# Optimization experiments

Measured on AMD Instinct MI355X. Metric: run time of the kernel, lower is better.

The kernel has to match this reference:

```python
import jax, jax.numpy as jnp
import numpy as np

B, S, HID = 1, 4096, 2048
H, KVH, D = 8, 4, 256
SW = 1024          # sliding window
EPS = 1e-6
NEG = -1e30


def _rmsnorm(x, w=None, eps=EPS):
    # torch nn.RMSNorm: x / sqrt(mean(x^2) + eps) * weight
    y = x * jax.lax.rsqrt(jnp.mean(x * x, axis=-1, keepdims=True) + eps)
    return y * w if w is not None else y


def _rotate_half(x):
    x1, x2 = jnp.split(x, 2, axis=-1)
    return jnp.concatenate([-x2, x1], axis=-1)


def _rope(x, cos, sin):
    # x: [B,S,H,D]; cos/sin: [B,S,rot] -> [B,S,1,rot]; rot == D here (no pass-through)
    c = cos[:, :, None, :]
    s = sin[:, :, None, :]
    return x * c + _rotate_half(x) * s


def setup_inputs() -> dict:
    key = jax.random.key(0)
    ks = jax.random.split(key, 9)
    return {
        "hidden_states": jax.random.normal(ks[0], (B, S, HID), jnp.float32),
        "cos": jax.random.uniform(ks[1], (B, S, D), jnp.float32),
        "sin": jax.random.uniform(ks[2], (B, S, D), jnp.float32),
        "q_w": jax.random.normal(ks[3], (H * D, HID), jnp.float32) * 0.02,
        "k_w": jax.random.normal(ks[4], (KVH * D, HID), jnp.float32) * 0.02,
        "v_w": jax.random.normal(ks[5], (KVH * D, HID), jnp.float32) * 0.02,
        "o_w": jax.random.normal(ks[6], (HID, H * D), jnp.float32) * 0.02,
        "q_norm_w": jnp.ones((D,), jnp.float32),
        "k_norm_w": jnp.ones((D,), jnp.float32),
    }


def reference(hidden_states, cos, sin, q_w, k_w, v_w, o_w, q_norm_w, k_norm_w):
    b, s, _ = hidden_states.shape
    # Projections (no bias), reshape to [B,S,heads,D]
    q = (hidden_states @ q_w.T).reshape(b, s, H, D)
    k = (hidden_states @ k_w.T).reshape(b, s, KVH, D)
    v = (hidden_states @ v_w.T).reshape(b, s, KVH, D)
    # per-head RMSNorm (v_norm has no affine), then RoPE on q/k
    q = _rope(_rmsnorm(q, q_norm_w), cos, sin)
    k = _rope(_rmsnorm(k, k_norm_w), cos, sin)
    v = _rmsnorm(v)
    # flatten(0,1): packed tokens T = B*S
    T = b * s
    q = q.reshape(T, H, D).transpose(1, 0, 2)          # [H,T,D]
    k = k.reshape(T, KVH, D).transpose(1, 0, 2)        # [KVH,T,D]
    v = v.reshape(T, KVH, D).transpose(1, 0, 2)
    # GQA: repeat_interleave kv heads
    rep = H // KVH
    k = jnp.repeat(k, rep, axis=0)                     # [H,T,D]
    v = jnp.repeat(v, rep, axis=0)
    # causal + sliding-window mask (allowed: i-SW < j <= i), scale=1.0
    i = jnp.arange(T)[:, None]
    j = jnp.arange(T)[None, :]
    allowed = (j <= i) & ((i - j) < SW)                # [T,T] bool
    scores = jnp.einsum("htd,hsd->hts", q, k)          # [H,T,T]
    scores = jnp.where(allowed[None], scores, NEG)
    p = jax.nn.softmax(scores, axis=-1)
    out = jnp.einsum("hts,hsd->htd", p, v)             # [H,T,D]
    out = out.transpose(1, 0, 2).reshape(b, s, H * D)
    return out @ o_w.T
```

## Files before the change

kernel.cpp:

```cpp
#include <hip/hip_runtime.h>
#include <stdint.h>

typedef __bf16 bf16x8 __attribute__((ext_vector_type(8)));
typedef __bf16 bf16x4 __attribute__((ext_vector_type(4)));
typedef _Float16 f16x8 __attribute__((ext_vector_type(8)));
typedef _Float16 f16x4 __attribute__((ext_vector_type(4)));
typedef float f32x4v __attribute__((ext_vector_type(4)));

__device__ __forceinline__ void async_copy16(const void* gptr, void* ldsptr) {
  __builtin_amdgcn_global_load_lds(
      (const __attribute__((address_space(1))) void*)gptr,
      (__attribute__((address_space(3))) void*)ldsptr,
      16, 0, 0);
}

__global__ __launch_bounds__(256) void cvt_split_f16(
    const float* __restrict__ src, _Float16* __restrict__ hi,
    _Float16* __restrict__ lo, int n4) {
  const int i = blockIdx.x * 256 + threadIdx.x;
  if (i < n4) {
    const float4 v = ((const float4*)src)[i];
    float vv[4] = {v.x, v.y, v.z, v.w};
    f16x4 h, l;
    for (int j = 0; j < 4; ++j) {
      h[j] = (_Float16)vv[j];
      l[j] = (_Float16)(vv[j] - (float)h[j]);
    }
    ((f16x4*)hi)[i] = h;
    ((f16x4*)lo)[i] = l;
  }
}

__global__ __launch_bounds__(256) void cvt_f16(
    const float* __restrict__ src, _Float16* __restrict__ hi, int n4) {
  const int i = blockIdx.x * 256 + threadIdx.x;
  if (i < n4) {
    const float4 v = ((const float4*)src)[i];
    f16x4 h = {(_Float16)v.x, (_Float16)v.y, (_Float16)v.z, (_Float16)v.w};
    ((f16x4*)hi)[i] = h;
  }
}

__global__ __launch_bounds__(256, 4) void gemm_qkv(
    const _Float16* __restrict__ Ah, const _Float16* __restrict__ Al,
    const _Float16* __restrict__ Bh, float* __restrict__ C) {
  const int K = 2048, ldc = 4096;
  __shared__ __align__(16) _Float16 Ash[128 * 32];
  __shared__ __align__(16) _Float16 Asl[128 * 32];
  __shared__ __align__(16) _Float16 Bsh[128 * 32];
  const int bid = blockIdx.x;
  const int xcd = bid & 7, c = bid >> 3;
  const int m0 = (c >> 2) * 128, n0 = (xcd * 4 + (c & 3)) * 128;
  const int tid = threadIdx.x;
  const int wid = tid >> 6, lane = tid & 63, l15 = lane & 15, quad = lane >> 4;
  const int wm = wid >> 1, wn = wid & 1;

  f32x4v acc[4][4] = {};

  for (int kb = 0; kb < K; kb += 32) {
    for (int it = 0; it < 2; ++it) {
      const int cc = (wid * 2 + it) * 64 + lane;
      const int row = cc >> 2;
      const int sc = (cc & 3) ^ ((row >> 1) & 3);
      const size_t ao = (size_t)(m0 + row) * K + kb + sc * 8;
      const size_t bo = (size_t)(n0 + row) * K + kb + sc * 8;
      const int dst = (wid * 2 + it) * 512;
      async_copy16(Ah + ao, &Ash[dst]);
      async_copy16(Al + ao, &Asl[dst]);
      async_copy16(Bh + bo, &Bsh[dst]);
    }
    __syncthreads();
    f16x8 afh[4], afl[4], bfh[4];
    for (int mt = 0; mt < 4; ++mt) {
      const int r = wm * 64 + mt * 16 + l15;
      const int o = r * 32 + ((quad ^ ((r >> 1) & 3)) * 8);
      afh[mt] = *(const f16x8*)&Ash[o];
      afl[mt] = *(const f16x8*)&Asl[o];
    }
    for (int nt = 0; nt < 4; ++nt) {
      const int r = wn * 64 + nt * 16 + l15;
      const int o = r * 32 + ((quad ^ ((r >> 1) & 3)) * 8);
      bfh[nt] = *(const f16x8*)&Bsh[o];
    }
    for (int mt = 0; mt < 4; ++mt)
      for (int nt = 0; nt < 4; ++nt) {
        acc[mt][nt] = __builtin_amdgcn_mfma_f32_16x16x32_f16(afh[mt], bfh[nt], acc[mt][nt], 0, 0, 0);
        acc[mt][nt] = __builtin_amdgcn_mfma_f32_16x16x32_f16(afl[mt], bfh[nt], acc[mt][nt], 0, 0, 0);
      }
    __syncthreads();
  }
  for (int mt = 0; mt < 4; ++mt)
    for (int nt = 0; nt < 4; ++nt) {
      const int row = m0 + wm * 64 + mt * 16 + quad * 4;
      const int col = n0 + wn * 64 + nt * 16 + l15;
      for (int r = 0; r < 4; ++r)
        C[(size_t)(row + r) * ldc + col] = acc[mt][nt][r];
    }
}

__global__ __launch_bounds__(64) void norm_rope(
    const float* __restrict__ qkv, const float* __restrict__ cosb,
    const float* __restrict__ sinb, const float* __restrict__ qnw,
    const float* __restrict__ knw,
    _Float16* __restrict__ qh, _Float16* __restrict__ ql,
    _Float16* __restrict__ kh, _Float16* __restrict__ vT) {
  const int s = blockIdx.x, c = blockIdx.y, lane = threadIdx.x;
  const int d0 = lane * 4;
  const float4 xv = *(const float4*)(qkv + (size_t)s * 4096 + c * 256 + d0);
  float v[4] = {xv.x, xv.y, xv.z, xv.w};
  float ss = v[0] * v[0] + v[1] * v[1] + v[2] * v[2] + v[3] * v[3];
  for (int off = 1; off < 64; off <<= 1) ss += __shfl_xor(ss, off);
  const float rn = rsqrtf(ss * (1.0f / 256.0f) + 1e-6f);
  if (c < 12) {
    const float* w = (c < 8) ? qnw : knw;
    float y[4], yp[4];
    for (int j = 0; j < 4; ++j) y[j] = v[j] * rn * w[d0 + j];
    for (int j = 0; j < 4; ++j) yp[j] = __shfl_xor(y[j], 32);
    for (int j = 0; j < 4; ++j) {
      const int d = d0 + j;
      const float rot = (d < 128) ? -yp[j] : yp[j];
      y[j] = y[j] * cosb[s * 256 + d] + rot * sinb[s * 256 + d];
    }
    if (c < 8) {
      const size_t o = ((size_t)c * 4096 + s) * 256 + d0;
      f16x4 hv, lv;
      for (int j = 0; j < 4; ++j) {
        hv[j] = (_Float16)y[j];
        lv[j] = (_Float16)(y[j] - (float)hv[j]);
      }
      *(f16x4*)(qh + o) = hv;
      *(f16x4*)(ql + o) = lv;
    } else {
      const size_t o = ((size_t)(c - 8) * 4096 + s) * 256 + d0;
      f16x4 hv;
      for (int j = 0; j < 4; ++j) hv[j] = (_Float16)y[j];
      *(f16x4*)(kh + o) = hv;
    }
  } else {
    const int kvh = c - 12;
    for (int j = 0; j < 4; ++j)
      vT[(size_t)(kvh * 256 + d0 + j) * 4096 + s] = (_Float16)(v[j] * rn);
  }
}

__global__ __launch_bounds__(512, 2) void attn_mfma(
    const _Float16* __restrict__ Qh_, const _Float16* __restrict__ Ql_,
    const _Float16* __restrict__ Kh_, const _Float16* __restrict__ VT,
    _Float16* __restrict__ Aout) {
  const int S = 4096, D = 256;
  const int bid = blockIdx.y * 32 + blockIdx.x;
  const int swz = (bid & 7) * 32 + (bid >> 3);
  const int h = swz >> 5;
  const int q0 = (swz & 31) * 128;
  const int tid = threadIdx.x;
  const int wid = tid >> 6, lane = tid & 63, l15 = lane & 15, quad = lane >> 4;
  const int kv = h >> 1;

  __shared__ __align__(16) _Float16 Ksh[2][32 * 256];
  __shared__ __align__(16) _Float16 Vs[2][256 * 32];
  __shared__ __align__(16) _Float16 P[8][16][32];

  const _Float16* Khh = Kh_ + (size_t)kv * S * D;
  const _Float16* Vh = VT + (size_t)kv * D * S;

  auto stage = [&](int buf, int kt) {
    for (int set = 0; set < 2; ++set) {
      const int n = set * 512 + wid * 64 + lane;
      const int row = n >> 5, c = n & 31;
      const int sc = c ^ (row & 7);
      const size_t go = (size_t)(kt + row) * D + sc * 8;
      const int dst = (set * 512 + wid * 64) * 8;
      async_copy16(Khh + go, &Ksh[buf][dst]);
      const int dim = n >> 2, kc = n & 3;
      const size_t vo = (size_t)dim * S + kt + (kc ^ ((dim >> 1) & 3)) * 8;
      async_copy16(Vh + vo, &Vs[buf][dst]);
    }
  };

  f16x8 qfh[8], qfl[8];
  {
    const size_t qoff =
        (size_t)h * S * D + (size_t)(q0 + wid * 16 + l15) * D + quad * 8;
    for (int ks = 0; ks < 8; ++ks) {
      qfh[ks] = *(const f16x8*)(Qh_ + qoff + ks * 32);
      qfl[ks] = *(const f16x8*)(Ql_ + qoff + ks * 32);
    }
  }

  f32x4v O[16] = {};
  float mrow[4] = {-1e30f, -1e30f, -1e30f, -1e30f};
  float lrow[4] = {0.f, 0.f, 0.f, 0.f};

  const int lo = (q0 >= 1024) ? (q0 - 1024) : 0;
  const int hi = q0 + 96;
  const int iqmin = q0 + wid * 16;
  const int iqmax = iqmin + 15;

  stage(0, lo);
  __syncthreads();
  int cur = 0;

  for (int kt = lo; kt <= hi; kt += 32) {
    if (kt + 32 <= hi) stage(cur ^ 1, kt + 32);
    const bool active = (kt <= iqmax) && (kt + 31 >= iqmin - 1023);
    if (active) {
      f32x4v sa[2] = {};
      for (int nt = 0; nt < 2; ++nt) {
        const int row = nt * 16 + l15;
        const int rxk = row & 7;
        for (int ks = 0; ks < 8; ++ks) {
          const int c = (ks * 4 + quad) ^ rxk;
          const f16x8 kh8 = *(const f16x8*)&Ksh[cur][row * 256 + c * 8];
          sa[nt] = __builtin_amdgcn_mfma_f32_16x16x32_f16(qfh[ks], kh8, sa[nt], 0, 0, 0);
          sa[nt] = __builtin_amdgcn_mfma_f32_16x16x32_f16(qfl[ks], kh8, sa[nt], 0, 0, 0);
        }
      }
      float al[4];
      for (int r = 0; r < 4; ++r) {
        const int i = q0 + wid * 16 + quad * 4 + r;
        float mx = -1e30f;
        for (int nt = 0; nt < 2; ++nt) {
          const int j = kt + nt * 16 + l15;
          const float svv = ((j <= i) && (i - j < 1024)) ? sa[nt][r] : -1e30f;
          sa[nt][r] = svv;
          mx = fmaxf(mx, svv);
        }
        for (int off = 1; off < 16; off <<= 1) mx = fmaxf(mx, __shfl_xor(mx, off));
        const float mn = fmaxf(mrow[r], mx);
        al[r] = __expf(mrow[r] - mn);
        float ps = 0.f;
        const int prow = quad * 4 + r;
        const int px = (prow >> 1) & 3;
        for (int nt = 0; nt < 2; ++nt) {
          const float p = (mn <= -1e29f) ? 0.f : __expf(sa[nt][r] - mn);
          const int pc = (nt * 2 + (l15 >> 3)) ^ px;
          P[wid][prow][pc * 8 + (l15 & 7)] = (_Float16)p;
          ps += p;
        }
        for (int off = 1; off < 16; off <<= 1) ps += __shfl_xor(ps, off);
        lrow[r] = lrow[r] * al[r] + ps;
        mrow[r] = mn;
      }
      for (int nt2 = 0; nt2 < 16; ++nt2)
        for (int r = 0; r < 4; ++r) O[nt2][r] *= al[r];
      __asm__ volatile("s_waitcnt lgkmcnt(0)" ::: "memory");
      __builtin_amdgcn_sched_barrier(0);
      const int prx = (l15 >> 1) & 3;
      const f16x8 pf = *(const f16x8*)&P[wid][l15][(quad ^ prx) * 8];
      for (int nt2 = 0; nt2 < 16; ++nt2) {
        const int dim = nt2 * 16 + l15;
        const int vq = quad ^ ((dim >> 1) & 3);
        const f16x8 vf = *(const f16x8*)&Vs[cur][(dim * 4 + vq) * 8];
        O[nt2] = __builtin_amdgcn_mfma_f32_16x16x32_f16(pf, vf, O[nt2], 0, 0, 0);
      }
    }
    __syncthreads();
    cur ^= 1;
  }
  for (int nt2 = 0; nt2 < 16; ++nt2)
    for (int r = 0; r < 4; ++r) {
      const float o = O[nt2][r] / lrow[r];
      Aout[(size_t)(q0 + wid * 16 + quad * 4 + r) * 2048 + h * 256 + nt2 * 16 + l15] = (_Float16)o;
    }
}

__global__ __launch_bounds__(256, 4) void gemm_out(
    const _Float16* __restrict__ A, const _Float16* __restrict__ B,
    float* __restrict__ C) {
  const int K = 2048, ldc = 2048;
  __shared__ __align__(16) _Float16 As[128 * 32];
  __shared__ __align__(16) _Float16 Bs[128 * 32];
  const int bid = blockIdx.x;
  const int xcd = bid & 7, c = bid >> 3;
  const int m0 = (c >> 1) * 128, n0 = (xcd * 2 + (c & 1)) * 128;
  const int tid = threadIdx.x;
  const int wid = tid >> 6, lane = tid & 63, l15 = lane & 15, quad = lane >> 4;
  const int wm = wid >> 1, wn = wid & 1;

  f32x4v acc[4][4] = {};

  for (int kb = 0; kb < K; kb += 32) {
    for (int it = 0; it < 2; ++it) {
      const int cc = (wid * 2 + it) * 64 + lane;
      const int row = cc >> 2;
      const int sc = (cc & 3) ^ ((row >> 1) & 3);
      const size_t ao = (size_t)(m0 + row) * K + kb + sc * 8;
      const size_t bo = (size_t)(n0 + row) * K + kb + sc * 8;
      const int dst = (wid * 2 + it) * 512;
      async_copy16(A + ao, &As[dst]);
      async_copy16(B + bo, &Bs[dst]);
    }
    __syncthreads();
    f16x8 af[4], bfr[4];
    for (int mt = 0; mt < 4; ++mt) {
      const int r = wm * 64 + mt * 16 + l15;
      af[mt] = *(const f16x8*)&As[r * 32 + ((quad ^ ((r >> 1) & 3)) * 8)];
    }
    for (int nt = 0; nt < 4; ++nt) {
      const int r = wn * 64 + nt * 16 + l15;
      bfr[nt] = *(const f16x8*)&Bs[r * 32 + ((quad ^ ((r >> 1) & 3)) * 8)];
    }
    for (int mt = 0; mt < 4; ++mt)
      for (int nt = 0; nt < 4; ++nt)
        acc[mt][nt] = __builtin_amdgcn_mfma_f32_16x16x32_f16(af[mt], bfr[nt], acc[mt][nt], 0, 0, 0);
    __syncthreads();
  }
  for (int mt = 0; mt < 4; ++mt)
    for (int nt = 0; nt < 4; ++nt) {
      const int row = m0 + wm * 64 + mt * 16 + quad * 4;
      const int col = n0 + wn * 64 + nt * 16 + l15;
      for (int r = 0; r < 4; ++r)
        C[(size_t)(row + r) * ldc + col] = acc[mt][nt][r];
    }
}

extern "C" void kernel_launch(void* const* d_in, const int* in_sizes, int n_in,
                              void* d_out, int out_size, void* d_ws, size_t ws_size,
                              hipStream_t stream) {
  const float* hidden = (const float*)d_in[0];
  const float* cosb   = (const float*)d_in[1];
  const float* sinb   = (const float*)d_in[2];
  const float* qw     = (const float*)d_in[3];
  const float* kw     = (const float*)d_in[4];
  const float* vw     = (const float*)d_in[5];
  const float* ow     = (const float*)d_in[6];
  const float* qnw    = (const float*)d_in[7];
  const float* knw    = (const float*)d_in[8];
  float* out = (float*)d_out;

  const size_t MB = 1048576;
  char* ws = (char*)d_ws;
  float*    qkvf = (float*)ws;
  _Float16* attn = (_Float16*)ws;
  _Float16* hh   = (_Float16*)(ws + 64 * MB);
  _Float16* hl   = (_Float16*)(ws + 80 * MB);
  _Float16* wh   = (_Float16*)(ws + 96 * MB);
  _Float16* qh   = (_Float16*)(ws + 64 * MB);
  _Float16* ql   = (_Float16*)(ws + 80 * MB);
  _Float16* kh   = (_Float16*)(ws + 96 * MB);
  _Float16* vT   = (_Float16*)(ws + 104 * MB);
  _Float16* owh  = (_Float16*)(ws + 112 * MB);

  cvt_split_f16<<<dim3(8192), 256, 0, stream>>>(hidden, hh, hl, 2097152);
  cvt_f16<<<dim3(4096), 256, 0, stream>>>(qw, wh, 1048576);
  cvt_f16<<<dim3(2048), 256, 0, stream>>>(kw, wh + 4194304, 524288);
  cvt_f16<<<dim3(2048), 256, 0, stream>>>(vw, wh + 6291456, 524288);
  cvt_f16<<<dim3(4096), 256, 0, stream>>>(ow, owh, 1048576);

  gemm_qkv<<<dim3(1024), 256, 0, stream>>>(hh, hl, wh, qkvf);
  norm_rope<<<dim3(4096, 16), 64, 0, stream>>>(qkvf, cosb, sinb, qnw, knw,
                                               qh, ql, kh, vT);
  attn_mfma<<<dim3(32, 8), 512, 0, stream>>>(qh, ql, kh, vT, attn);
  gemm_out<<<dim3(512), 256, 0, stream>>>(attn, owh, out);
}
```

Before: 479.8 us.

## Shrink attention tiles to 64 queries, merge weight casts, widen norm blocks

```diff
diff --git a/kernel.cpp b/kernel.cpp
--- a/kernel.cpp
+++ b/kernel.cpp
@@ -2,7 +2,6 @@
 #include <stdint.h>
 
 typedef __bf16 bf16x8 __attribute__((ext_vector_type(8)));
-typedef __bf16 bf16x4 __attribute__((ext_vector_type(4)));
 typedef _Float16 f16x8 __attribute__((ext_vector_type(8)));
 typedef _Float16 f16x4 __attribute__((ext_vector_type(4)));
 typedef float f32x4v __attribute__((ext_vector_type(4)));
@@ -31,14 +30,21 @@
   }
 }
 
-__global__ __launch_bounds__(256) void cvt_f16(
-    const float* __restrict__ src, _Float16* __restrict__ hi, int n4) {
-  const int i = blockIdx.x * 256 + threadIdx.x;
-  if (i < n4) {
-    const float4 v = ((const float4*)src)[i];
-    f16x4 h = {(_Float16)v.x, (_Float16)v.y, (_Float16)v.z, (_Float16)v.w};
-    ((f16x4*)hi)[i] = h;
-  }
+__global__ __launch_bounds__(256) void cvt_weights(
+    const float* __restrict__ qw, const float* __restrict__ kw,
+    const float* __restrict__ vw, const float* __restrict__ ow,
+    _Float16* __restrict__ wh, _Float16* __restrict__ owh) {
+  const int b = blockIdx.x, tid = threadIdx.x;
+  const float* src;
+  _Float16* dst;
+  int i;
+  if (b < 4096)      { src = qw; dst = wh;           i = b * 256 + tid; }
+  else if (b < 6144) { src = kw; dst = wh + 4194304; i = (b - 4096) * 256 + tid; }
+  else if (b < 8192) { src = vw; dst = wh + 6291456; i = (b - 6144) * 256 + tid; }
+  else               { src = ow; dst = owh;          i = (b - 8192) * 256 + tid; }
+  const float4 v = ((const float4*)src)[i];
+  f16x4 h = {(_Float16)v.x, (_Float16)v.y, (_Float16)v.z, (_Float16)v.w};
+  ((f16x4*)dst)[i] = h;
 }
 
 __global__ __launch_bounds__(256, 4) void gemm_qkv(
@@ -98,13 +104,15 @@
     }
 }
 
-__global__ __launch_bounds__(64) void norm_rope(
+__global__ __launch_bounds__(256) void norm_rope(
     const float* __restrict__ qkv, const float* __restrict__ cosb,
     const float* __restrict__ sinb, const float* __restrict__ qnw,
     const float* __restrict__ knw,
     _Float16* __restrict__ qh, _Float16* __restrict__ ql,
     _Float16* __restrict__ kh, _Float16* __restrict__ vT) {
-  const int s = blockIdx.x, c = blockIdx.y, lane = threadIdx.x;
+  const int s = blockIdx.x;
+  const int wid = threadIdx.x >> 6, lane = threadIdx.x & 63;
+  const int c = blockIdx.y * 4 + wid;
   const int d0 = lane * 4;
   const float4 xv = *(const float4*)(qkv + (size_t)s * 4096 + c * 256 + d0);
   float v[4] = {xv.x, xv.y, xv.z, xv.w};
@@ -143,33 +151,32 @@
   }
 }
 
-__global__ __launch_bounds__(512, 2) void attn_mfma(
+__global__ __launch_bounds__(256, 2) void attn_mfma(
     const _Float16* __restrict__ Qh_, const _Float16* __restrict__ Ql_,
     const _Float16* __restrict__ Kh_, const _Float16* __restrict__ VT,
     _Float16* __restrict__ Aout) {
   const int S = 4096, D = 256;
-  const int bid = blockIdx.y * 32 + blockIdx.x;
-  const int swz = (bid & 7) * 32 + (bid >> 3);
-  const int h = swz >> 5;
-  const int q0 = (swz & 31) * 128;
+  const int x = blockIdx.x, y = blockIdx.y;
+  const int h = x & 7;
+  const int q0 = (y * 8 + (x >> 3)) * 64;
   const int tid = threadIdx.x;
   const int wid = tid >> 6, lane = tid & 63, l15 = lane & 15, quad = lane >> 4;
   const int kv = h >> 1;
 
   __shared__ __align__(16) _Float16 Ksh[2][32 * 256];
   __shared__ __align__(16) _Float16 Vs[2][256 * 32];
-  __shared__ __align__(16) _Float16 P[8][16][32];
+  __shared__ __align__(16) _Float16 P[4][16][32];
 
   const _Float16* Khh = Kh_ + (size_t)kv * S * D;
   const _Float16* Vh = VT + (size_t)kv * D * S;
 
   auto stage = [&](int buf, int kt) {
-    for (int set = 0; set < 2; ++set) {
-      const int n = set * 512 + wid * 64 + lane;
+    for (int set = 0; set < 4; ++set) {
+      const int n = set * 256 + wid * 64 + lane;
       const int row = n >> 5, c = n & 31;
       const int sc = c ^ (row & 7);
       const size_t go = (size_t)(kt + row) * D + sc * 8;
-      const int dst = (set * 512 + wid * 64) * 8;
+      const int dst = (set * 256 + wid * 64) * 8;
       async_copy16(Khh + go, &Ksh[buf][dst]);
       const int dim = n >> 2, kc = n & 3;
       const size_t vo = (size_t)dim * S + kt + (kc ^ ((dim >> 1) & 3)) * 8;
@@ -192,7 +199,7 @@
   float lrow[4] = {0.f, 0.f, 0.f, 0.f};
 
   const int lo = (q0 >= 1024) ? (q0 - 1024) : 0;
-  const int hi = q0 + 96;
+  const int hi = q0 + 32;
   const int iqmin = q0 + wid * 16;
   const int iqmax = iqmin + 15;
 
@@ -342,14 +349,11 @@
   _Float16* owh  = (_Float16*)(ws + 112 * MB);
 
   cvt_split_f16<<<dim3(8192), 256, 0, stream>>>(hidden, hh, hl, 2097152);
-  cvt_f16<<<dim3(4096), 256, 0, stream>>>(qw, wh, 1048576);
-  cvt_f16<<<dim3(2048), 256, 0, stream>>>(kw, wh + 4194304, 524288);
-  cvt_f16<<<dim3(2048), 256, 0, stream>>>(vw, wh + 6291456, 524288);
-  cvt_f16<<<dim3(4096), 256, 0, stream>>>(ow, owh, 1048576);
+  cvt_weights<<<dim3(12288), 256, 0, stream>>>(qw, kw, vw, ow, wh, owh);
 
   gemm_qkv<<<dim3(1024), 256, 0, stream>>>(hh, hl, wh, qkvf);
-  norm_rope<<<dim3(4096, 16), 64, 0, stream>>>(qkvf, cosb, sinb, qnw, knw,
+  norm_rope<<<dim3(4096, 4), 256, 0, stream>>>(qkvf, cosb, sinb, qnw, knw,
                                                qh, ql, kh, vT);
-  attn_mfma<<<dim3(32, 8), 512, 0, stream>>>(qh, ql, kh, vT, attn);
+  attn_mfma<<<dim3(64, 8), 256, 0, stream>>>(qh, ql, kh, vT, attn);
   gemm_out<<<dim3(512), 256, 0, stream>>>(attn, owh, out);
 }
```

Measured after the change: 473.9 us. Within noise of the previous version (-1.2%).
